# Performance work log

Hardware: AMD Instinct MI355X
Metric: run time of the kernel (lower is better)

The kernel has to match this reference:

```python
import jax, jax.numpy as jnp
import numpy as np

N = 50000      # nodes
E = 800000     # edges (avg degree 16)
F_IN = 256     # input feature dim
H = 4          # heads
D = 16         # out feats per head
NEG_SLOPE = 0.2


def setup_inputs() -> dict:
    key = jax.random.key(0)
    ks = jax.random.split(key, 8)
    feat = jax.random.normal(ks[0], (N, F_IN), dtype=jnp.float32)
    src = jax.random.randint(ks[1], (E,), 0, N, dtype=jnp.int32)
    dst = jax.random.randint(ks[2], (E,), 0, N, dtype=jnp.int32)
    sc = 1.0 / np.sqrt(F_IN)
    W_src = (jax.random.normal(ks[3], (H * D, F_IN), dtype=jnp.float32) * sc)
    b_src = jnp.zeros((H * D,), dtype=jnp.float32)
    W_dst = (jax.random.normal(ks[4], (H * D, F_IN), dtype=jnp.float32) * sc)
    b_dst = jnp.zeros((H * D,), dtype=jnp.float32)
    attn = jax.random.normal(ks[5], (1, H, D), dtype=jnp.float32) * (1.0 / np.sqrt(D))
    return {"feat": feat, "src": src, "dst": dst, "W_src": W_src,
            "b_src": b_src, "W_dst": W_dst, "b_dst": b_dst, "attn": attn}


def reference(feat, src, dst, W_src, b_src, W_dst, b_dst, attn):
    # Dense projections: [N, H, D]
    feat_src = (feat @ W_src.T + b_src).reshape(N, H, D)
    feat_dst = (feat @ W_dst.T + b_dst).reshape(N, H, D)
    # Gather to edges: [E, H, D]
    el = feat_src[src]
    er = feat_dst[dst]
    e = jax.nn.leaky_relu(el + er, negative_slope=NEG_SLOPE)
    # Per-edge, per-head attention logit: [E, H]
    score = jnp.einsum('ehd,ohd->eh', e, attn)
    # Edge softmax over incoming edges of each destination node
    m = jax.ops.segment_max(score, dst, num_segments=N)          # [N, H]
    a = jnp.exp(score - m[dst])                                  # [E, H]
    s = jax.ops.segment_sum(a, dst, num_segments=N)              # [N, H]
    alpha = a / s[dst]                                           # [E, H]
    # Weighted scatter-aggregate of source features: [N, H, D]
    msg = el * alpha[:, :, None]
    rst = jax.ops.segment_sum(msg, dst, num_segments=N)
    return rst
```

## Files before the change

kernel.cpp:

```cpp
#include <hip/hip_runtime.h>
#include <math.h>

#define NODES 50000
#define EDGES 800000
#define FIN   256
#define HD    64
#define NEG   0.2f

#define PROJ_BLOCKS 782
#define NB          196
#define STAGE_BLOCKS 196
#define PREP_BLOCKS 128

typedef __attribute__((ext_vector_type(8))) short bf16x8;
typedef __attribute__((ext_vector_type(4))) float f32x4;

__device__ __forceinline__ unsigned pack_hi(unsigned a, unsigned b)
{ return (a >> 16) | (b & 0xFFFF0000u); }

__device__ __forceinline__ void split8(const float4 x01, const float4 x23,
                                       bf16x8& hi, bf16x8& lo)
{
    const float xs[8] = { x01.x, x01.y, x01.z, x01.w, x23.x, x23.y, x23.z, x23.w };
    union { unsigned w[4]; bf16x8 v; } H, L;
#pragma unroll
    for (int p = 0; p < 4; ++p) {
        const float a = xs[2 * p], b = xs[2 * p + 1];
        const unsigned ba = __float_as_uint(a), bb = __float_as_uint(b);
        H.w[p] = pack_hi(ba, bb);
        const float la = a - __uint_as_float(ba & 0xFFFF0000u);
        const float lb = b - __uint_as_float(bb & 0xFFFF0000u);
        L.w[p] = pack_hi(__float_as_uint(la), __float_as_uint(lb));
    }
    hi = H.v; lo = L.v;
}

__global__ void prep_count_kernel(const float* __restrict__ Wsrc,
                                  const float* __restrict__ Wdst,
                                  short* __restrict__ Bhi, short* __restrict__ Blo,
                                  const int* __restrict__ dst, int* __restrict__ bcnt)
{
    const int b = blockIdx.x;
    const int t = threadIdx.x;
    if (b < PREP_BLOCKS) {
        const int i = b * 256 + t;
        const int row = i >> 8, k = i & 255;
        const float x = (row < 64) ? Wsrc[row * FIN + k] : Wdst[(row - 64) * FIN + k];
        const unsigned bb = __float_as_uint(x);
        const float l = x - __uint_as_float(bb & 0xFFFF0000u);
        Bhi[i] = (short)(bb >> 16);
        Blo[i] = (short)(__float_as_uint(l) >> 16);
        return;
    }
    __shared__ int sH[NB];
    for (int i = t; i < NB; i += 256) sH[i] = 0;
    __syncthreads();
    const int e0 = (b - PREP_BLOCKS) * 4096;
#pragma unroll
    for (int k = 0; k < 16; ++k) {
        const int e = e0 + k * 256 + t;
        if (e < EDGES) atomicAdd(&sH[dst[e] >> 8], 1);
    }
    __syncthreads();
    for (int i = t; i < NB; i += 256) {
        const int c = sH[i];
        if (c) atomicAdd(&bcnt[i], c);
    }
}

__global__ void bscan_kernel(const int* __restrict__ bcnt, int* __restrict__ bbase,
                             int* __restrict__ bcur, int* __restrict__ offs)
{
    __shared__ int s[256];
    const int t = threadIdx.x;
    const int v = (t < NB) ? bcnt[t] : 0;
    s[t] = v;
    __syncthreads();
    for (int off = 1; off < 256; off <<= 1) {
        const int x = (t >= off) ? s[t - off] : 0;
        __syncthreads();
        s[t] += x;
        __syncthreads();
    }
    const int excl = s[t] - v;
    if (t <= NB) bbase[t] = excl;
    if (t < NB)  bcur[t]  = excl;
    if (t == 0)  offs[NODES] = EDGES;
}

__global__ __launch_bounds__(256) void proj_stage_kernel(
    const float* __restrict__ feat,
    const short* __restrict__ Bhi, const short* __restrict__ Blo,
    const float* __restrict__ bsrc, const float* __restrict__ bdst,
    float* __restrict__ fs, float* __restrict__ fd,
    const int* __restrict__ src, const int* __restrict__ dst,
    int* __restrict__ bcur, unsigned* __restrict__ bedge)
{
    __shared__ short sB[2][2][512 * 8];
    __shared__ int   sH[NB], sBase[NB];

    const int t = threadIdx.x;

    if (blockIdx.x >= PROJ_BLOCKS) {
        const int e0 = (blockIdx.x - PROJ_BLOCKS) * 4096;
        for (int i = t; i < NB; i += 256) sH[i] = 0;
        __syncthreads();
#pragma unroll
        for (int k = 0; k < 16; ++k) {
            const int e = e0 + k * 256 + t;
            if (e < EDGES) atomicAdd(&sH[dst[e] >> 8], 1);
        }
        __syncthreads();
        for (int i = t; i < NB; i += 256) {
            const int c = sH[i];
            sBase[i] = c ? atomicAdd(&bcur[i], c) : 0;
            sH[i] = 0;
        }
        __syncthreads();
#pragma unroll
        for (int k = 0; k < 16; ++k) {
            const int e = e0 + k * 256 + t;
            if (e < EDGES) {
                const int d = dst[e];
                const int b = d >> 8;
                const int p = sBase[b] + atomicAdd(&sH[b], 1);
                bedge[p] = (unsigned)src[e] | ((unsigned)(d & 255) << 16);
            }
        }
        return;
    }

    const int lane = t & 63;
    const int w    = t >> 6;
    const int fr   = lane & 15;
    const int fq   = lane >> 4;
    const int fragu = fq * 128 + fr;

    const int colu = t & 127;
    const int fq0  = t >> 7;
    const int fq1  = fq0 + 2;

    const int r0 = blockIdx.x * 64 + w * 16;
    int rowA = r0 + fr;  if (rowA >= NODES) rowA = NODES - 1;
    const float* pA = feat + (size_t)rowA * FIN + fq * 8;

    f32x4 acc[8];
#pragma unroll
    for (int n = 0; n < 8; ++n) acc[n] = (f32x4){0.f, 0.f, 0.f, 0.f};

    float4 bs00, bs01, bs10, bs11;
    float4 aR[3][2];

#define B_ISSUE(kslice) do {                                                  \
        const size_t o0 = (size_t)colu * FIN + (kslice) * 32 + fq0 * 8;       \
        const size_t o1 = (size_t)colu * FIN + (kslice) * 32 + fq1 * 8;       \
        bs00 = *(const float4*)(Bhi + o0);  bs01 = *(const float4*)(Bhi + o1);\
        bs10 = *(const float4*)(Blo + o0);  bs11 = *(const float4*)(Blo + o1);\
    } while (0)

#define B_WRITE(buf) do {                                                     \
        *(float4*)&sB[buf][0][(size_t)t * 8]         = bs00;                  \
        *(float4*)&sB[buf][0][(size_t)(t + 256) * 8] = bs01;                  \
        *(float4*)&sB[buf][1][(size_t)t * 8]         = bs10;                  \
        *(float4*)&sB[buf][1][(size_t)(t + 256) * 8] = bs11;                  \
    } while (0)

#define A_LD(r, kslice) do {                                                  \
        aR[r][0] = *(const float4*)(pA + (kslice) * 32);                      \
        aR[r][1] = *(const float4*)(pA + (kslice) * 32 + 4);                  \
    } while (0)

#define COMPUTE(buf, AH, AL) do {                                             \
        _Pragma("unroll")                                                     \
        for (int nf = 0; nf < 8; ++nf) {                                      \
            const bf16x8 bh = *(const bf16x8*)&sB[buf][0][(fragu + nf*16)*8]; \
            const bf16x8 bl = *(const bf16x8*)&sB[buf][1][(fragu + nf*16)*8]; \
            acc[nf] = __builtin_amdgcn_mfma_f32_16x16x32_bf16(AH, bh, acc[nf], 0, 0, 0); \
            acc[nf] = __builtin_amdgcn_mfma_f32_16x16x32_bf16(AL, bh, acc[nf], 0, 0, 0); \
            acc[nf] = __builtin_amdgcn_mfma_f32_16x16x32_bf16(AH, bl, acc[nf], 0, 0, 0); \
        } } while (0)

    B_ISSUE(0);
    A_LD(0, 0);
    A_LD(1, 1);
    B_WRITE(0);
    __syncthreads();

#pragma unroll
    for (int ks = 0; ks < 8; ++ks) {
        const int buf = ks & 1;
        if (ks < 7) B_ISSUE(ks + 1);
        if (ks < 6) A_LD((ks + 2) % 3, ks + 2);
        bf16x8 ah, al;
        split8(aR[ks % 3][0], aR[ks % 3][1], ah, al);
        COMPUTE(buf, ah, al);
        if (ks < 7) B_WRITE(buf ^ 1);
        __syncthreads();
    }

#pragma unroll
    for (int nf = 0; nf < 8; ++nf) {
        float* outp = (nf < 4) ? fs : fd;
        const float bias = ((nf < 4) ? bsrc : bdst)[(nf & 3) * 16 + fr];
        const int c = (nf & 3) * 16 + fr;
#pragma unroll
        for (int r = 0; r < 4; ++r) {
            const int row = r0 + fq * 4 + r;
            if (row < NODES)
                outp[(size_t)row * HD + c] = acc[nf][r] + bias;
        }
    }
#undef B_ISSUE
#undef B_WRITE
#undef A_LD
#undef COMPUTE
}

__global__ __launch_bounds__(256) void bucket_scatter_kernel(
    const int* __restrict__ bbase, const unsigned* __restrict__ bedge,
    int* __restrict__ offs, unsigned short* __restrict__ csr)
{
    __shared__ int s[256];
    __shared__ int pl[256];
    const int b = blockIdx.x;
    const int t = threadIdx.x;
    const int start = bbase[b];
    const int end   = bbase[b + 1];

    s[t] = 0;
    __syncthreads();
    for (int i = start + t; i < end; i += 256)
        atomicAdd(&s[(bedge[i] >> 16) & 255], 1);
    __syncthreads();

    const int v = s[t];
    __syncthreads();
    for (int off = 1; off < 256; off <<= 1) {
        const int x = (t >= off) ? s[t - off] : 0;
        __syncthreads();
        s[t] += x;
        __syncthreads();
    }
    const int excl = s[t] - v;

    const int node = b * 256 + t;
    if (node < NODES) offs[node] = start + excl;
    pl[t] = excl;
    __syncthreads();

    for (int i = start + t; i < end; i += 256) {
        const unsigned pk = bedge[i];
        const int rel = atomicAdd(&pl[(pk >> 16) & 255], 1);
        csr[start + rel] = (unsigned short)(pk & 0xFFFFu);
    }
}

__device__ __forceinline__ float head_sum16(float x)
{
    x += __int_as_float(__builtin_amdgcn_update_dpp(0, __float_as_int(x), 0xB1,  0xf, 0xf, true));
    x += __int_as_float(__builtin_amdgcn_update_dpp(0, __float_as_int(x), 0x4E,  0xf, 0xf, true));
    x += __int_as_float(__builtin_amdgcn_update_dpp(0, __float_as_int(x), 0x141, 0xf, 0xf, true));
    x += __int_as_float(__builtin_amdgcn_update_dpp(0, __float_as_int(x), 0x140, 0xf, 0xf, true));
    return x;
}

__global__ __launch_bounds__(256) void gat_kernel(
    const float* __restrict__ fs, const float* __restrict__ fd,
    const float* __restrict__ attn,
    const int* __restrict__ offs, const unsigned short* __restrict__ csr,
    float* __restrict__ out)
{
    const int wid  = (blockIdx.x * blockDim.x + threadIdx.x) >> 6;
    const int lane = threadIdx.x & 63;
    if (wid >= NODES) return;

    const float er = fd[(size_t)wid * HD + lane];
    const float aw = attn[lane];
    const int start = __builtin_amdgcn_readfirstlane(offs[wid]);
    const int end   = __builtin_amdgcn_readfirstlane(offs[wid + 1]);

    float s = 0.f, acc = 0.f;

    for (int base = start; base < end; base += 64) {
        const int rem = end - base;
        const int cnt = rem < 64 ? rem : 64;
        int srcv = 0;
        if (lane < cnt) srcv = (int)csr[base + lane];

        int j = 0;
        for (; j + 4 <= cnt; j += 4) {
            const int i0 = __builtin_amdgcn_readlane(srcv, j + 0);
            const int i1 = __builtin_amdgcn_readlane(srcv, j + 1);
            const int i2 = __builtin_amdgcn_readlane(srcv, j + 2);
            const int i3 = __builtin_amdgcn_readlane(srcv, j + 3);
            const float el0 = fs[(size_t)i0 * HD + lane];
            const float el1 = fs[(size_t)i1 * HD + lane];
            const float el2 = fs[(size_t)i2 * HD + lane];
            const float el3 = fs[(size_t)i3 * HD + lane];
            const float t0 = el0 + er, t1 = el1 + er, t2 = el2 + er, t3 = el3 + er;
            const float e0 = fmaf(NEG, fminf(t0, 0.f), fmaxf(t0, 0.f));
            const float e1 = fmaf(NEG, fminf(t1, 0.f), fmaxf(t1, 0.f));
            const float e2 = fmaf(NEG, fminf(t2, 0.f), fmaxf(t2, 0.f));
            const float e3 = fmaf(NEG, fminf(t3, 0.f), fmaxf(t3, 0.f));
            const float p0 = head_sum16(e0 * aw);
            const float p1 = head_sum16(e1 * aw);
            const float p2 = head_sum16(e2 * aw);
            const float p3 = head_sum16(e3 * aw);
            const float pe0 = __expf(p0);
            const float pe1 = __expf(p1);
            const float pe2 = __expf(p2);
            const float pe3 = __expf(p3);
            s += (pe0 + pe1) + (pe2 + pe3);
            acc = fmaf(pe0, el0, fmaf(pe1, el1, fmaf(pe2, el2, fmaf(pe3, el3, acc))));
        }
        for (; j < cnt; ++j) {
            const int i0 = __builtin_amdgcn_readlane(srcv, j);
            const float el0 = fs[(size_t)i0 * HD + lane];
            const float t0 = el0 + er;
            const float e0 = fmaf(NEG, fminf(t0, 0.f), fmaxf(t0, 0.f));
            const float pe0 = __expf(head_sum16(e0 * aw));
            s += pe0;
            acc = fmaf(pe0, el0, acc);
        }
    }
    out[(size_t)wid * HD + lane] = (end > start) ? (acc / s) : 0.f;
}

extern "C" void kernel_launch(void* const* d_in, const int* in_sizes, int n_in,
                              void* d_out, int out_size, void* d_ws, size_t ws_size,
                              hipStream_t stream)
{
    const float* feat = (const float*)d_in[0];
    const int*   src  = (const int*)  d_in[1];
    const int*   dst  = (const int*)  d_in[2];
    const float* Wsrc = (const float*)d_in[3];
    const float* bsrc = (const float*)d_in[4];
    const float* Wdst = (const float*)d_in[5];
    const float* bdst = (const float*)d_in[6];
    const float* attn = (const float*)d_in[7];
    float* out = (float*)d_out;

    float* fs     = (float*)d_ws;
    float* fd     = fs + (size_t)NODES * HD;
    int*   offs   = (int*)(fd + (size_t)NODES * HD);
    int*   bcnt   = offs + (NODES + 16);
    int*   bbase  = bcnt + 256;
    int*   bcur   = bbase + 256;
    unsigned* bedge = (unsigned*)(bcur + 256);
    unsigned short* csr = (unsigned short*)(bedge + EDGES);
    short* Bhi    = (short*)(csr + EDGES);
    short* Blo    = Bhi + 128 * FIN;

    hipMemsetAsync(bcnt, 0, 256 * sizeof(int), stream);

    prep_count_kernel<<<PREP_BLOCKS + STAGE_BLOCKS, 256, 0, stream>>>(
        Wsrc, Wdst, Bhi, Blo, dst, bcnt);
    bscan_kernel<<<1, 256, 0, stream>>>(bcnt, bbase, bcur, offs);
    proj_stage_kernel<<<PROJ_BLOCKS + STAGE_BLOCKS, 256, 0, stream>>>(
        feat, Bhi, Blo, bsrc, bdst, fs, fd, src, dst, bcur, bedge);
    bucket_scatter_kernel<<<NB, 256, 0, stream>>>(bbase, bedge, offs, csr);
    gat_kernel<<<((size_t)NODES * 64 + 255) / 256, 256, 0, stream>>>(
        fs, fd, attn, offs, csr, out);
}
```

Baseline: 194.6 us.

## Split projection GEMM columns across two blocks and preload weights into LDS

The projection kernel now launches two blocks per 64-row tile, each computing either the src or dst half (64 output columns) instead of all 128. Each block loads its entire 64x256 hi/lo bf16 weight slice into shared memory once up front, which removes the per-k-slice double-buffered B staging and the barriers inside the k loop. This doubles parallelism and halves accumulator registers, at the cost of reading each feat row twice from global memory and using more shared memory per block (64 KB), which may limit occupancy.

```diff
diff --git a/kernel.cpp b/kernel.cpp
--- a/kernel.cpp
+++ b/kernel.cpp
@@ -7,10 +7,10 @@
 #define HD    64
 #define NEG   0.2f
 
-#define PROJ_BLOCKS 782
 #define NB          196
 #define STAGE_BLOCKS 196
 #define PREP_BLOCKS 128
+#define PROJ_BLOCKS2 1564
 
 typedef __attribute__((ext_vector_type(8))) short bf16x8;
 typedef __attribute__((ext_vector_type(4))) float f32x4;
@@ -96,13 +96,13 @@
     const int* __restrict__ src, const int* __restrict__ dst,
     int* __restrict__ bcur, unsigned* __restrict__ bedge)
 {
-    __shared__ short sB[2][2][512 * 8];
+    __shared__ short sB[2][2048 * 8];
     __shared__ int   sH[NB], sBase[NB];
 
     const int t = threadIdx.x;
 
-    if (blockIdx.x >= PROJ_BLOCKS) {
-        const int e0 = (blockIdx.x - PROJ_BLOCKS) * 4096;
+    if (blockIdx.x >= PROJ_BLOCKS2) {
+        const int e0 = (blockIdx.x - PROJ_BLOCKS2) * 4096;
         for (int i = t; i < NB; i += 256) sH[i] = 0;
         __syncthreads();
 #pragma unroll
@@ -130,90 +130,72 @@
         return;
     }
 
+    const int half = blockIdx.x & 1;
+    const int tile = blockIdx.x >> 1;
     const int lane = t & 63;
     const int w    = t >> 6;
     const int fr   = lane & 15;
     const int fq   = lane >> 4;
-    const int fragu = fq * 128 + fr;
-
-    const int colu = t & 127;
-    const int fq0  = t >> 7;
-    const int fq1  = fq0 + 2;
-
-    const int r0 = blockIdx.x * 64 + w * 16;
+
+    const short* Bh = Bhi + (size_t)half * 64 * FIN;
+    const short* Bl = Blo + (size_t)half * 64 * FIN;
+
+    const int r0 = tile * 64 + w * 16;
     int rowA = r0 + fr;  if (rowA >= NODES) rowA = NODES - 1;
     const float* pA = feat + (size_t)rowA * FIN + fq * 8;
 
-    f32x4 acc[8];
-#pragma unroll
-    for (int n = 0; n < 8; ++n) acc[n] = (f32x4){0.f, 0.f, 0.f, 0.f};
-
-    float4 bs00, bs01, bs10, bs11;
     float4 aR[3][2];
-
-#define B_ISSUE(kslice) do {                                                  \
-        const size_t o0 = (size_t)colu * FIN + (kslice) * 32 + fq0 * 8;       \
-        const size_t o1 = (size_t)colu * FIN + (kslice) * 32 + fq1 * 8;       \
-        bs00 = *(const float4*)(Bhi + o0);  bs01 = *(const float4*)(Bhi + o1);\
-        bs10 = *(const float4*)(Blo + o0);  bs11 = *(const float4*)(Blo + o1);\
-    } while (0)
-
-#define B_WRITE(buf) do {                                                     \
-        *(float4*)&sB[buf][0][(size_t)t * 8]         = bs00;                  \
-        *(float4*)&sB[buf][0][(size_t)(t + 256) * 8] = bs01;                  \
-        *(float4*)&sB[buf][1][(size_t)t * 8]         = bs10;                  \
-        *(float4*)&sB[buf][1][(size_t)(t + 256) * 8] = bs11;                  \
-    } while (0)
-
-#define A_LD(r, kslice) do {                                                  \
-        aR[r][0] = *(const float4*)(pA + (kslice) * 32);                      \
-        aR[r][1] = *(const float4*)(pA + (kslice) * 32 + 4);                  \
-    } while (0)
-
-#define COMPUTE(buf, AH, AL) do {                                             \
-        _Pragma("unroll")                                                     \
-        for (int nf = 0; nf < 8; ++nf) {                                      \
-            const bf16x8 bh = *(const bf16x8*)&sB[buf][0][(fragu + nf*16)*8]; \
-            const bf16x8 bl = *(const bf16x8*)&sB[buf][1][(fragu + nf*16)*8]; \
-            acc[nf] = __builtin_amdgcn_mfma_f32_16x16x32_bf16(AH, bh, acc[nf], 0, 0, 0); \
-            acc[nf] = __builtin_amdgcn_mfma_f32_16x16x32_bf16(AL, bh, acc[nf], 0, 0, 0); \
-            acc[nf] = __builtin_amdgcn_mfma_f32_16x16x32_bf16(AH, bl, acc[nf], 0, 0, 0); \
-        } } while (0)
-
-    B_ISSUE(0);
-    A_LD(0, 0);
-    A_LD(1, 1);
-    B_WRITE(0);
-    __syncthreads();
+    aR[0][0] = *(const float4*)(pA);       aR[0][1] = *(const float4*)(pA + 4);
+    aR[1][0] = *(const float4*)(pA + 32);  aR[1][1] = *(const float4*)(pA + 36);
+
+#pragma unroll
+    for (int j = 0; j < 8; ++j) {
+        const int u   = t + j * 256;
+        const int s   = u >> 8;
+        const int fqq = (u >> 6) & 3;
+        const int c   = u & 63;
+        const size_t go = (size_t)c * FIN + s * 32 + fqq * 8;
+        *(float4*)&sB[0][(size_t)u * 8] = *(const float4*)(Bh + go);
+        *(float4*)&sB[1][(size_t)u * 8] = *(const float4*)(Bl + go);
+    }
+    __syncthreads();
+
+    f32x4 acc[4];
+#pragma unroll
+    for (int n = 0; n < 4; ++n) acc[n] = (f32x4){0.f, 0.f, 0.f, 0.f};
 
 #pragma unroll
     for (int ks = 0; ks < 8; ++ks) {
-        const int buf = ks & 1;
-        if (ks < 7) B_ISSUE(ks + 1);
-        if (ks < 6) A_LD((ks + 2) % 3, ks + 2);
+        if (ks < 6) {
+            aR[(ks + 2) % 3][0] = *(const float4*)(pA + (ks + 2) * 32);
+            aR[(ks + 2) % 3][1] = *(const float4*)(pA + (ks + 2) * 32 + 4);
+        }
         bf16x8 ah, al;
         split8(aR[ks % 3][0], aR[ks % 3][1], ah, al);
-        COMPUTE(buf, ah, al);
-        if (ks < 7) B_WRITE(buf ^ 1);
-        __syncthreads();
-    }
-
-#pragma unroll
-    for (int nf = 0; nf < 8; ++nf) {
-        float* outp = (nf < 4) ? fs : fd;
-        const float bias = ((nf < 4) ? bsrc : bdst)[(nf & 3) * 16 + fr];
-        const int c = (nf & 3) * 16 + fr;
+#pragma unroll
+        for (int nf = 0; nf < 4; ++nf) {
+            const int u = (ks * 4 + fq) * 64 + nf * 16 + fr;
+            const bf16x8 bh = *(const bf16x8*)&sB[0][(size_t)u * 8];
+            const bf16x8 bl = *(const bf16x8*)&sB[1][(size_t)u * 8];
+            acc[nf] = __builtin_amdgcn_mfma_f32_16x16x32_bf16(ah, bh, acc[nf], 0, 0, 0);
+            acc[nf] = __builtin_amdgcn_mfma_f32_16x16x32_bf16(al, bh, acc[nf], 0, 0, 0);
+            acc[nf] = __builtin_amdgcn_mfma_f32_16x16x32_bf16(ah, bl, acc[nf], 0, 0, 0);
+        }
+    }
+
+    const float* bias = half ? bdst : bsrc;
+    float* outp = half ? fd : fs;
+#pragma unroll
+    for (int nf = 0; nf < 4; ++nf) {
+        const int c = nf * 16 + fr;
+        const float bv = bias[c];
 #pragma unroll
         for (int r = 0; r < 4; ++r) {
             const int row = r0 + fq * 4 + r;
             if (row < NODES)
-                outp[(size_t)row * HD + c] = acc[nf][r] + bias;
-        }
-    }
-#undef B_ISSUE
-#undef B_WRITE
-#undef A_LD
-#undef COMPUTE
+                outp[(size_t)row * HD + c] = acc[nf][r] + bv;
+        }
+    }
 }
 
 __global__ __launch_bounds__(256) void bucket_scatter_kernel(
@@ -356,7 +338,7 @@
     prep_count_kernel<<<PREP_BLOCKS + STAGE_BLOCKS, 256, 0, stream>>>(
         Wsrc, Wdst, Bhi, Blo, dst, bcnt);
     bscan_kernel<<<1, 256, 0, stream>>>(bcnt, bbase, bcur, offs);
-    proj_stage_kernel<<<PROJ_BLOCKS + STAGE_BLOCKS, 256, 0, stream>>>(
+    proj_stage_kernel<<<PROJ_BLOCKS2 + STAGE_BLOCKS, 256, 0, stream>>>(
         feat, Bhi, Blo, bsrc, bdst, fs, fd, src, dst, bcur, bedge);
     bucket_scatter_kernel<<<NB, 256, 0, stream>>>(bbase, bedge, offs, csr);
     gat_kernel<<<((size_t)NODES * 64 + 255) / 256, 256, 0, stream>>>(
```

After: 205.4 us. +5.6%, slower.
